# Performance work log

Hardware: AMD Instinct MI355X
Metric: run time of the kernel (lower is better)

Reference implementation:

```python
import jax, jax.numpy as jnp
import numpy as np

D_MODEL = 1024
N_HEADS = 16


def setup_inputs() -> dict:
    key = jax.random.key(0)
    ks = jax.random.split(key, 11)
    B, S, D = 2, 2048, D_MODEL
    scale = 1.0 / np.sqrt(D)
    inp = {
        "q": jax.random.normal(ks[0], (B, S, D), jnp.float32),
        "k": jax.random.normal(ks[1], (B, S, D), jnp.float32),
        "v": jax.random.normal(ks[2], (B, S, D), jnp.float32),
        "W_q": jax.random.normal(ks[3], (D, D), jnp.float32) * scale,
        "b_q": jnp.zeros((D,), jnp.float32),
        "W_k": jax.random.normal(ks[4], (D, D), jnp.float32) * scale,
        "b_k": jnp.zeros((D,), jnp.float32),
        "W_v": jax.random.normal(ks[5], (D, D), jnp.float32) * scale,
        "b_v": jnp.zeros((D,), jnp.float32),
        "W_o": jax.random.normal(ks[6], (D, D), jnp.float32) * scale,
        "b_o": jnp.zeros((D,), jnp.float32),
    }
    return inp


def reference(q, k, v, W_q, b_q, W_k, b_k, W_v, b_v, W_o, b_o):
    B, S, D = q.shape
    H = N_HEADS
    d_k = D // H
    # linear projections, then split heads: [B, H, S, d_k]
    def proj(x, W, b):
        y = jnp.einsum("bsd,de->bse", x, W.T) + b
        return y.reshape(B, S, H, d_k).transpose(0, 2, 1, 3)
    Q = proj(q, W_q, b_q)
    K = proj(k, W_k, b_k)
    V = proj(v, W_v, b_v)
    # scaled dot-product attention with explicit [B,H,S,S] scores
    scores = jnp.einsum("bhqd,bhkd->bhqk", Q, K) / jnp.sqrt(jnp.float32(d_k))
    attn = jax.nn.softmax(scores, axis=-1)
    out = jnp.einsum("bhqk,bhkd->bhqd", attn, V)
    out = out.transpose(0, 2, 1, 3).reshape(B, S, D)
    return jnp.einsum("bsd,de->bse", out, W_o.T) + b_o
```

## Files before the change

kernel.cpp:

```cpp
#include <hip/hip_runtime.h>
#include <hip/hip_bf16.h>
#include <math.h>

typedef __bf16 bf16_t;
typedef bf16_t bf16x8 __attribute__((ext_vector_type(8)));
typedef float f32x4 __attribute__((ext_vector_type(4)));

#define D_MODEL 1024
#define NH 16
#define DK 64
#define SEQ 2048
#define MROWS 4096
#define LDP 72
#define LDSW 64
#define LDC 136

__device__ __forceinline__ bf16x8 ldfrag(const bf16_t* p) {
    union { uint4 u; bf16x8 v; } c;
    c.u = *reinterpret_cast<const uint4*>(p);
    return c.v;
}

__device__ __forceinline__ f32x4 zero4() { f32x4 z = {0.f, 0.f, 0.f, 0.f}; return z; }

__device__ __forceinline__ void gll16(const bf16_t* g, bf16_t* l) {
    __builtin_amdgcn_global_load_lds(
        (const __attribute__((address_space(1))) unsigned int*)g,
        (__attribute__((address_space(3))) unsigned int*)l,
        16, 0, 0);
}

__global__ void pack3(const float* __restrict__ a, const float* __restrict__ b,
                      const float* __restrict__ c,
                      bf16_t* __restrict__ da, bf16_t* __restrict__ db, bf16_t* __restrict__ dc) {
    const float* s = (blockIdx.y == 0) ? a : (blockIdx.y == 1) ? b : c;
    bf16_t* d      = (blockIdx.y == 0) ? da : (blockIdx.y == 1) ? db : dc;
    int i = (blockIdx.x * blockDim.x + threadIdx.x) * 4;
    float4 f = *reinterpret_cast<const float4*>(s + i);
    union { bf16_t h[4]; uint2 u; } o;
    o.h[0] = (bf16_t)f.x; o.h[1] = (bf16_t)f.y; o.h[2] = (bf16_t)f.z; o.h[3] = (bf16_t)f.w;
    *reinterpret_cast<uint2*>(d + i) = o.u;
}

__global__ void pack4(const float* __restrict__ a, const float* __restrict__ b,
                      const float* __restrict__ c, const float* __restrict__ e,
                      bf16_t* __restrict__ da, bf16_t* __restrict__ db,
                      bf16_t* __restrict__ dc, bf16_t* __restrict__ de) {
    const float* s = (blockIdx.y == 0) ? a : (blockIdx.y == 1) ? b : (blockIdx.y == 2) ? c : e;
    bf16_t* d      = (blockIdx.y == 0) ? da : (blockIdx.y == 1) ? db : (blockIdx.y == 2) ? dc : de;
    int i = (blockIdx.x * blockDim.x + threadIdx.x) * 4;
    float4 f = *reinterpret_cast<const float4*>(s + i);
    union { bf16_t h[4]; uint2 u; } o;
    o.h[0] = (bf16_t)f.x; o.h[1] = (bf16_t)f.y; o.h[2] = (bf16_t)f.z; o.h[3] = (bf16_t)f.w;
    *reinterpret_cast<uint2*>(d + i) = o.u;
}

__device__ __forceinline__ void gemm_core(
    const bf16_t* __restrict__ A, const bf16_t* __restrict__ Bm,
    int K, int m0, int n0,
    bf16_t* As, bf16_t* Bs,
    f32x4 acc[4][4]) {

    const int tid = threadIdx.x;
    const int lane = tid & 63;
    const int wid = tid >> 6;
    const int wm = (wid >> 1) * 64, wn = (wid & 1) * 64;
    const int l15 = lane & 15, quad = lane >> 4;

    const int lrow   = lane >> 3;
    const int gcol   = ((lane & 7) ^ lrow) * 8;

    #pragma unroll
    for (int i = 0; i < 4; i++)
        #pragma unroll
        for (int j = 0; j < 4; j++) acc[i][j] = zero4();

    for (int k0 = 0; k0 < K; k0 += 64) {
        __syncthreads();
        #pragma unroll
        for (int t = 0; t < 4; t++) {
            const int rbase = wid * 32 + t * 8;
            gll16(A  + (size_t)(m0 + rbase + lrow) * K + k0 + gcol, As + rbase * LDSW);
            gll16(Bm + (size_t)(n0 + rbase + lrow) * K + k0 + gcol, Bs + rbase * LDSW);
        }
        __syncthreads();
        #pragma unroll
        for (int c = 0; c < 2; c++) {
            bf16x8 af[4], bfr[4];
            #pragma unroll
            for (int i = 0; i < 4; i++) {
                const int row = wm + i * 16 + l15;
                const int pc = ((c * 4 + quad) ^ (l15 & 7)) * 8;
                af[i] = ldfrag(As + row * LDSW + pc);
            }
            #pragma unroll
            for (int j = 0; j < 4; j++) {
                const int row = wn + j * 16 + l15;
                const int pc = ((c * 4 + quad) ^ (l15 & 7)) * 8;
                bfr[j] = ldfrag(Bs + row * LDSW + pc);
            }
            #pragma unroll
            for (int i = 0; i < 4; i++)
                #pragma unroll
                for (int j = 0; j < 4; j++)
                    acc[i][j] = __builtin_amdgcn_mfma_f32_16x16x32_bf16(af[i], bfr[j], acc[i][j], 0, 0, 0);
        }
    }
}

__global__ __launch_bounds__(256, 2) void proj_gemm(
    const bf16_t* __restrict__ qb, const bf16_t* __restrict__ kb,
    const bf16_t* __restrict__ vb,
    const bf16_t* __restrict__ Wq, const bf16_t* __restrict__ Wk,
    const bf16_t* __restrict__ Wv,
    const float* __restrict__ bq, const float* __restrict__ bk, const float* __restrict__ bv,
    bf16_t* __restrict__ Qh, bf16_t* __restrict__ Kh, bf16_t* __restrict__ Vt) {

    __shared__ __align__(16) bf16_t sm[128 * LDC];
    bf16_t* As = sm;
    bf16_t* Bs = sm + 128 * LDSW;
    bf16_t (*Cs)[LDC] = reinterpret_cast<bf16_t(*)[LDC]>(sm);
    f32x4 acc[4][4];

    const int mode = blockIdx.z;
    const bf16_t* X = (mode == 0) ? qb : (mode == 1) ? kb : vb;
    const bf16_t* W = (mode == 0) ? Wq : (mode == 1) ? Wk : Wv;
    const float* bias = (mode == 0) ? bq : (mode == 1) ? bk : bv;
    const int m0 = blockIdx.y * 128, n0 = blockIdx.x * 128;

    gemm_core(X, W, D_MODEL, m0, n0, As, Bs, acc);

    const int tid = threadIdx.x, lane = tid & 63, wid = tid >> 6;
    const int wm = (wid >> 1) * 64, wn = (wid & 1) * 64;
    const int l15 = lane & 15, quad = lane >> 4;

    __syncthreads();
    if (mode != 2) {
        const float sc = (mode == 0) ? 0.125f * 1.44269504f : 1.0f;
        #pragma unroll
        for (int i = 0; i < 4; i++)
            #pragma unroll
            for (int j = 0; j < 4; j++)
                #pragma unroll
                for (int r = 0; r < 4; r++) {
                    int gn = n0 + wn + j * 16 + l15;
                    Cs[wm + i * 16 + quad * 4 + r][wn + j * 16 + l15] =
                        (bf16_t)((acc[i][j][r] + bias[gn]) * sc);
                }
    } else {
        #pragma unroll
        for (int i = 0; i < 4; i++)
            #pragma unroll
            for (int j = 0; j < 4; j++)
                #pragma unroll
                for (int r = 0; r < 4; r++) {
                    int gn = n0 + wn + j * 16 + l15;
                    Cs[wn + j * 16 + l15][wm + i * 16 + quad * 4 + r] =
                        (bf16_t)(acc[i][j][r] + bias[gn]);
                }
    }
    __syncthreads();

    #pragma unroll
    for (int c = tid; c < 2048; c += 256) {
        int row = c >> 4, col8 = (c & 15) << 3;
        uint4 val = *reinterpret_cast<const uint4*>(&Cs[row][col8]);
        if (mode != 2) {
            int gm = m0 + row, gn = n0 + col8;
            int b = gm >> 11, seq = gm & 2047;
            int h = gn >> 6, dk = gn & 63;
            bf16_t* dst = (mode == 0) ? Qh : Kh;
            *reinterpret_cast<uint4*>(dst + ((size_t)(b * NH + h) * SEQ + seq) * DK + dk) = val;
        } else {
            int gn = n0 + row, gm = m0 + col8;
            int b = gm >> 11, seq = gm & 2047;
            int h = gn >> 6, dk = gn & 63;
            *reinterpret_cast<uint4*>(Vt + ((size_t)(b * NH + h) * DK + dk) * SEQ + seq) = val;
        }
    }
}

__global__ __launch_bounds__(256, 2) void out_gemm(
    const bf16_t* __restrict__ Oc, const bf16_t* __restrict__ Wo,
    const float* __restrict__ bo, float* __restrict__ Cout) {

    __shared__ __align__(16) bf16_t As[128 * LDSW];
    __shared__ __align__(16) bf16_t Bs[128 * LDSW];
    f32x4 acc[4][4];
    const int m0 = blockIdx.y * 128, n0 = blockIdx.x * 128;

    gemm_core(Oc, Wo, D_MODEL, m0, n0, As, Bs, acc);

    const int tid = threadIdx.x, lane = tid & 63, wid = tid >> 6;
    const int wm = (wid >> 1) * 64, wn = (wid & 1) * 64;
    const int l15 = lane & 15, quad = lane >> 4;

    #pragma unroll
    for (int i = 0; i < 4; i++)
        #pragma unroll
        for (int j = 0; j < 4; j++)
            #pragma unroll
            for (int r = 0; r < 4; r++) {
                int gm = m0 + wm + i * 16 + quad * 4 + r;
                int gn = n0 + wn + j * 16 + l15;
                Cout[(size_t)gm * D_MODEL + gn] = acc[i][j][r] + bo[gn];
            }
}

__global__ __launch_bounds__(256) void attn_kernel(
    const bf16_t* __restrict__ Qh, const bf16_t* __restrict__ Kh,
    const bf16_t* __restrict__ Vt, bf16_t* __restrict__ Oc) {

    __shared__ __align__(16) bf16_t Ks[64 * LDSW];
    __shared__ __align__(16) bf16_t Vts[64 * LDSW];
    __shared__ __align__(16) bf16_t Pls[64][LDP];

    const int tid = threadIdx.x, lane = tid & 63, wid = tid >> 6;
    const int l15 = lane & 15, quad = lane >> 4;
    const int bh = blockIdx.x;
    const int q0 = blockIdx.y * 64;
    const bf16_t* Qbase = Qh + (size_t)bh * SEQ * DK;
    const bf16_t* Kbase = Kh + (size_t)bh * SEQ * DK;
    const bf16_t* Vbase = Vt + (size_t)bh * DK * SEQ;

    const int lrow = lane >> 3;
    const int gcol = ((lane & 7) ^ lrow) * 8;

    bf16x8 aQ[2];
    #pragma unroll
    for (int c = 0; c < 2; c++)
        aQ[c] = ldfrag(Qbase + (size_t)(q0 + wid * 16 + l15) * DK + c * 32 + quad * 8);

    f32x4 oacc[4];
    #pragma unroll
    for (int j = 0; j < 4; j++) oacc[j] = zero4();
    float l_i[4] = {0.f, 0.f, 0.f, 0.f};

    for (int kt = 0; kt < SEQ / 64; kt++) {
        const int k0 = kt * 64;
        __syncthreads();
        #pragma unroll
        for (int t = 0; t < 2; t++) {
            const int rbase = wid * 16 + t * 8;
            gll16(Kbase + (size_t)(k0 + rbase + lrow) * DK + gcol,  Ks  + rbase * LDSW);
            gll16(Vbase + (size_t)(rbase + lrow) * SEQ + k0 + gcol, Vts + rbase * LDSW);
        }
        __syncthreads();

        f32x4 sacc[4];
        #pragma unroll
        for (int j = 0; j < 4; j++) sacc[j] = zero4();
        #pragma unroll
        for (int c = 0; c < 2; c++) {
            bf16x8 bk4[4];
            #pragma unroll
            for (int j = 0; j < 4; j++) {
                const int pc = ((c * 4 + quad) ^ (l15 & 7)) * 8;
                bk4[j] = ldfrag(Ks + (j * 16 + l15) * LDSW + pc);
            }
            #pragma unroll
            for (int j = 0; j < 4; j++)
                sacc[j] = __builtin_amdgcn_mfma_f32_16x16x32_bf16(
                    aQ[c], bk4[j], sacc[j], 0, 0, 0);
        }

        #pragma unroll
        for (int r = 0; r < 4; r++) {
            float e0 = exp2f(sacc[0][r]);
            float e1 = exp2f(sacc[1][r]);
            float e2 = exp2f(sacc[2][r]);
            float e3 = exp2f(sacc[3][r]);
            l_i[r] += (e0 + e1) + (e2 + e3);
            bf16_t* prow = &Pls[wid * 16 + quad * 4 + r][0];
            prow[l15]      = (bf16_t)e0;
            prow[16 + l15] = (bf16_t)e1;
            prow[32 + l15] = (bf16_t)e2;
            prow[48 + l15] = (bf16_t)e3;
        }

        #pragma unroll
        for (int c = 0; c < 2; c++) {
            bf16x8 ap = ldfrag(&Pls[wid * 16 + l15][c * 32 + quad * 8]);
            bf16x8 bv4[4];
            #pragma unroll
            for (int j = 0; j < 4; j++) {
                const int pc = ((c * 4 + quad) ^ (l15 & 7)) * 8;
                bv4[j] = ldfrag(Vts + (j * 16 + l15) * LDSW + pc);
            }
            #pragma unroll
            for (int j = 0; j < 4; j++)
                oacc[j] = __builtin_amdgcn_mfma_f32_16x16x32_bf16(
                    ap, bv4[j], oacc[j], 0, 0, 0);
        }
    }

    #pragma unroll
    for (int r = 0; r < 4; r++) {
        float l = l_i[r];
        #pragma unroll
        for (int off = 1; off < 16; off <<= 1)
            l += __shfl_xor(l, off, 64);
        float inv = 1.0f / l;
        #pragma unroll
        for (int j = 0; j < 4; j++)
            Pls[wid * 16 + quad * 4 + r][j * 16 + l15] = (bf16_t)(oacc[j][r] * inv);
    }
    __syncthreads();

    const int b = bh >> 4, h = bh & 15;
    #pragma unroll
    for (int c = tid; c < 512; c += 256) {
        int row = c >> 3, col8 = (c & 7) << 3;
        uint4 val = *reinterpret_cast<const uint4*>(&Pls[row][col8]);
        *reinterpret_cast<uint4*>(Oc + ((size_t)(b * SEQ + q0 + row)) * D_MODEL + h * DK + col8) = val;
    }
}

extern "C" void kernel_launch(void* const* d_in, const int* in_sizes, int n_in,
                              void* d_out, int out_size, void* d_ws, size_t ws_size,
                              hipStream_t stream) {
    const float* q  = (const float*)d_in[0];
    const float* k  = (const float*)d_in[1];
    const float* v  = (const float*)d_in[2];
    const float* Wq = (const float*)d_in[3];
    const float* bq = (const float*)d_in[4];
    const float* Wk = (const float*)d_in[5];
    const float* bk = (const float*)d_in[6];
    const float* Wv = (const float*)d_in[7];
    const float* bv = (const float*)d_in[8];
    const float* Wo = (const float*)d_in[9];
    const float* bo = (const float*)d_in[10];

    const size_t nx = (size_t)MROWS * D_MODEL;
    const size_t nw = (size_t)D_MODEL * D_MODEL;

    bf16_t* qb  = (bf16_t*)d_ws;
    bf16_t* kb  = qb  + nx;
    bf16_t* vb  = kb  + nx;
    bf16_t* Wqb = vb  + nx;
    bf16_t* Wkb = Wqb + nw;
    bf16_t* Wvb = Wkb + nw;
    bf16_t* Wob = Wvb + nw;
    bf16_t* Qh  = Wob + nw;
    bf16_t* Kh  = Qh  + nx;
    bf16_t* Vt  = Kh  + nx;
    bf16_t* Oc  = Vt  + nx;

    pack3<<<dim3(4096, 3), 256, 0, stream>>>(q, k, v, qb, kb, vb);
    pack4<<<dim3(1024, 4), 256, 0, stream>>>(Wq, Wk, Wv, Wo, Wqb, Wkb, Wvb, Wob);

    proj_gemm<<<dim3(8, 32, 3), 256, 0, stream>>>(qb, kb, vb, Wqb, Wkb, Wvb, bq, bk, bv, Qh, Kh, Vt);
    attn_kernel<<<dim3(32, 32), 256, 0, stream>>>(Qh, Kh, Vt, Oc);
    out_gemm<<<dim3(8, 32), 256, 0, stream>>>(Oc, Wob, bo, (float*)d_out);
}
```

Baseline: 250.2 us.

## Double-buffer LDS tiles in GEMMs and attention; swizzle P staging buffer

```diff
diff --git a/kernel.cpp b/kernel.cpp
--- a/kernel.cpp
+++ b/kernel.cpp
@@ -11,7 +11,6 @@
 #define DK 64
 #define SEQ 2048
 #define MROWS 4096
-#define LDP 72
 #define LDSW 64
 #define LDC 136
 
@@ -75,15 +74,26 @@
         #pragma unroll
         for (int j = 0; j < 4; j++) acc[i][j] = zero4();
 
-    for (int k0 = 0; k0 < K; k0 += 64) {
+    #pragma unroll
+    for (int t = 0; t < 4; t++) {
+        const int rbase = wid * 32 + t * 8;
+        gll16(A  + (size_t)(m0 + rbase + lrow) * K + gcol, As + rbase * LDSW);
+        gll16(Bm + (size_t)(n0 + rbase + lrow) * K + gcol, Bs + rbase * LDSW);
+    }
+
+    int kt = 0;
+    for (int k0 = 0; k0 < K; k0 += 64, kt++) {
         __syncthreads();
-        #pragma unroll
-        for (int t = 0; t < 4; t++) {
-            const int rbase = wid * 32 + t * 8;
-            gll16(A  + (size_t)(m0 + rbase + lrow) * K + k0 + gcol, As + rbase * LDSW);
-            gll16(Bm + (size_t)(n0 + rbase + lrow) * K + k0 + gcol, Bs + rbase * LDSW);
-        }
-        __syncthreads();
+        const int cur = (kt & 1) * 128 * LDSW;
+        if (k0 + 64 < K) {
+            const int nxt = ((kt + 1) & 1) * 128 * LDSW;
+            #pragma unroll
+            for (int t = 0; t < 4; t++) {
+                const int rbase = wid * 32 + t * 8;
+                gll16(A  + (size_t)(m0 + rbase + lrow) * K + k0 + 64 + gcol, As + nxt + rbase * LDSW);
+                gll16(Bm + (size_t)(n0 + rbase + lrow) * K + k0 + 64 + gcol, Bs + nxt + rbase * LDSW);
+            }
+        }
         #pragma unroll
         for (int c = 0; c < 2; c++) {
             bf16x8 af[4], bfr[4];
@@ -91,13 +101,13 @@
             for (int i = 0; i < 4; i++) {
                 const int row = wm + i * 16 + l15;
                 const int pc = ((c * 4 + quad) ^ (l15 & 7)) * 8;
-                af[i] = ldfrag(As + row * LDSW + pc);
+                af[i] = ldfrag(As + cur + row * LDSW + pc);
             }
             #pragma unroll
             for (int j = 0; j < 4; j++) {
                 const int row = wn + j * 16 + l15;
                 const int pc = ((c * 4 + quad) ^ (l15 & 7)) * 8;
-                bfr[j] = ldfrag(Bs + row * LDSW + pc);
+                bfr[j] = ldfrag(Bs + cur + row * LDSW + pc);
             }
             #pragma unroll
             for (int i = 0; i < 4; i++)
@@ -116,9 +126,9 @@
     const float* __restrict__ bq, const float* __restrict__ bk, const float* __restrict__ bv,
     bf16_t* __restrict__ Qh, bf16_t* __restrict__ Kh, bf16_t* __restrict__ Vt) {
 
-    __shared__ __align__(16) bf16_t sm[128 * LDC];
+    __shared__ __align__(16) bf16_t sm[4 * 128 * LDSW];
     bf16_t* As = sm;
-    bf16_t* Bs = sm + 128 * LDSW;
+    bf16_t* Bs = sm + 2 * 128 * LDSW;
     bf16_t (*Cs)[LDC] = reinterpret_cast<bf16_t(*)[LDC]>(sm);
     f32x4 acc[4][4];
 
@@ -184,8 +194,8 @@
     const bf16_t* __restrict__ Oc, const bf16_t* __restrict__ Wo,
     const float* __restrict__ bo, float* __restrict__ Cout) {
 
-    __shared__ __align__(16) bf16_t As[128 * LDSW];
-    __shared__ __align__(16) bf16_t Bs[128 * LDSW];
+    __shared__ __align__(16) bf16_t As[2 * 128 * LDSW];
+    __shared__ __align__(16) bf16_t Bs[2 * 128 * LDSW];
     f32x4 acc[4][4];
     const int m0 = blockIdx.y * 128, n0 = blockIdx.x * 128;
 
@@ -211,9 +221,9 @@
     const bf16_t* __restrict__ Qh, const bf16_t* __restrict__ Kh,
     const bf16_t* __restrict__ Vt, bf16_t* __restrict__ Oc) {
 
-    __shared__ __align__(16) bf16_t Ks[64 * LDSW];
-    __shared__ __align__(16) bf16_t Vts[64 * LDSW];
-    __shared__ __align__(16) bf16_t Pls[64][LDP];
+    __shared__ __align__(16) bf16_t Ks[2 * 64 * LDSW];
+    __shared__ __align__(16) bf16_t Vts[2 * 64 * LDSW];
+    __shared__ __align__(16) bf16_t Pls[64 * LDSW];
 
     const int tid = threadIdx.x, lane = tid & 63, wid = tid >> 6;
     const int l15 = lane & 15, quad = lane >> 4;
@@ -236,16 +246,26 @@
     for (int j = 0; j < 4; j++) oacc[j] = zero4();
     float l_i[4] = {0.f, 0.f, 0.f, 0.f};
 
+    #pragma unroll
+    for (int t = 0; t < 2; t++) {
+        const int rbase = wid * 16 + t * 8;
+        gll16(Kbase + (size_t)(rbase + lrow) * DK + gcol,  Ks  + rbase * LDSW);
+        gll16(Vbase + (size_t)(rbase + lrow) * SEQ + gcol, Vts + rbase * LDSW);
+    }
+
     for (int kt = 0; kt < SEQ / 64; kt++) {
-        const int k0 = kt * 64;
         __syncthreads();
-        #pragma unroll
-        for (int t = 0; t < 2; t++) {
-            const int rbase = wid * 16 + t * 8;
-            gll16(Kbase + (size_t)(k0 + rbase + lrow) * DK + gcol,  Ks  + rbase * LDSW);
-            gll16(Vbase + (size_t)(rbase + lrow) * SEQ + k0 + gcol, Vts + rbase * LDSW);
-        }
-        __syncthreads();
+        const int cur = (kt & 1) * 64 * LDSW;
+        if (kt + 1 < SEQ / 64) {
+            const int k1 = (kt + 1) * 64;
+            const int nxt = ((kt + 1) & 1) * 64 * LDSW;
+            #pragma unroll
+            for (int t = 0; t < 2; t++) {
+                const int rbase = wid * 16 + t * 8;
+                gll16(Kbase + (size_t)(k1 + rbase + lrow) * DK + gcol,  Ks  + nxt + rbase * LDSW);
+                gll16(Vbase + (size_t)(rbase + lrow) * SEQ + k1 + gcol, Vts + nxt + rbase * LDSW);
+            }
+        }
 
         f32x4 sacc[4];
         #pragma unroll
@@ -256,7 +276,7 @@
             #pragma unroll
             for (int j = 0; j < 4; j++) {
                 const int pc = ((c * 4 + quad) ^ (l15 & 7)) * 8;
-                bk4[j] = ldfrag(Ks + (j * 16 + l15) * LDSW + pc);
+                bk4[j] = ldfrag(Ks + cur + (j * 16 + l15) * LDSW + pc);
             }
             #pragma unroll
             for (int j = 0; j < 4; j++)
@@ -271,21 +291,25 @@
             float e2 = exp2f(sacc[2][r]);
             float e3 = exp2f(sacc[3][r]);
             l_i[r] += (e0 + e1) + (e2 + e3);
-            bf16_t* prow = &Pls[wid * 16 + quad * 4 + r][0];
-            prow[l15]      = (bf16_t)e0;
-            prow[16 + l15] = (bf16_t)e1;
-            prow[32 + l15] = (bf16_t)e2;
-            prow[48 + l15] = (bf16_t)e3;
+            const int prow = wid * 16 + quad * 4 + r;
+            bf16_t* pbase = Pls + prow * LDSW;
+            const int hi = l15 >> 3, lo = l15 & 7, sw = prow & 7;
+            pbase[((0 + hi) ^ sw) * 8 + lo] = (bf16_t)e0;
+            pbase[((2 + hi) ^ sw) * 8 + lo] = (bf16_t)e1;
+            pbase[((4 + hi) ^ sw) * 8 + lo] = (bf16_t)e2;
+            pbase[((6 + hi) ^ sw) * 8 + lo] = (bf16_t)e3;
         }
 
         #pragma unroll
         for (int c = 0; c < 2; c++) {
-            bf16x8 ap = ldfrag(&Pls[wid * 16 + l15][c * 32 + quad * 8]);
+            const int prow = wid * 16 + l15;
+            const int ppc = ((c * 4 + quad) ^ (l15 & 7)) * 8;
+            bf16x8 ap = ldfrag(Pls + prow * LDSW + ppc);
             bf16x8 bv4[4];
             #pragma unroll
             for (int j = 0; j < 4; j++) {
                 const int pc = ((c * 4 + quad) ^ (l15 & 7)) * 8;
-                bv4[j] = ldfrag(Vts + (j * 16 + l15) * LDSW + pc);
+                bv4[j] = ldfrag(Vts + cur + (j * 16 + l15) * LDSW + pc);
             }
             #pragma unroll
             for (int j = 0; j < 4; j++)
@@ -301,18 +325,21 @@
         for (int off = 1; off < 16; off <<= 1)
             l += __shfl_xor(l, off, 64);
         float inv = 1.0f / l;
+        const int prow = wid * 16 + quad * 4 + r;
+        bf16_t* pbase = Pls + prow * LDSW;
+        const int hi = l15 >> 3, lo = l15 & 7, sw = prow & 7;
         #pragma unroll
         for (int j = 0; j < 4; j++)
-            Pls[wid * 16 + quad * 4 + r][j * 16 + l15] = (bf16_t)(oacc[j][r] * inv);
+            pbase[((2 * j + hi) ^ sw) * 8 + lo] = (bf16_t)(oacc[j][r] * inv);
     }
     __syncthreads();
 
     const int b = bh >> 4, h = bh & 15;
     #pragma unroll
     for (int c = tid; c < 512; c += 256) {
-        int row = c >> 3, col8 = (c & 7) << 3;
-        uint4 val = *reinterpret_cast<const uint4*>(&Pls[row][col8]);
-        *reinterpret_cast<uint4*>(Oc + ((size_t)(b * SEQ + q0 + row)) * D_MODEL + h * DK + col8) = val;
+        int row = c >> 3, col8 = c & 7;
+        uint4 val = *reinterpret_cast<const uint4*>(Pls + row * LDSW + ((col8 ^ (row & 7)) << 3));
+        *reinterpret_cast<uint4*>(Oc + ((size_t)(b * SEQ + q0 + row)) * D_MODEL + h * DK + (col8 << 3)) = val;
     }
 }
 
```

Result: slower. 264.8 us (+5.8%).
